# Kernel tuning notes

Measured on AMD Instinct MI355X. Metric: run time of the kernel, lower is better.

The kernel has to match this reference:

```python
import jax, jax.numpy as jnp
import numpy as np

INPUT_SIZE = 20
HIDDEN = 51
OUT = 1
B = 4096
T = 512


def _init_lstm_params(key, in_dim, hid_dim):
    # PyTorch LSTMCell init: U(-1/sqrt(hid), 1/sqrt(hid))
    k = 1.0 / np.sqrt(hid_dim)
    ks = jax.random.split(key, 4)
    W_ih = jax.random.uniform(ks[0], (4 * hid_dim, in_dim), minval=-k, maxval=k, dtype=jnp.float32)
    W_hh = jax.random.uniform(ks[1], (4 * hid_dim, hid_dim), minval=-k, maxval=k, dtype=jnp.float32)
    b_ih = jax.random.uniform(ks[2], (4 * hid_dim,), minval=-k, maxval=k, dtype=jnp.float32)
    b_hh = jax.random.uniform(ks[3], (4 * hid_dim,), minval=-k, maxval=k, dtype=jnp.float32)
    return W_ih, W_hh, b_ih, b_hh


def setup_inputs() -> dict:
    key = jax.random.key(0)
    k_x, k1, k2, k3, k4 = jax.random.split(key, 5)
    x = jax.random.normal(k_x, (B, T, INPUT_SIZE), dtype=jnp.float32)
    W_ih1, W_hh1, b_ih1, b_hh1 = _init_lstm_params(k1, INPUT_SIZE, HIDDEN)
    W_ih2, W_hh2, b_ih2, b_hh2 = _init_lstm_params(k2, HIDDEN, OUT)
    kl = 1.0 / np.sqrt(OUT)
    ka, kb, kc, kd = jax.random.split(k3, 4)
    W_mu = jax.random.uniform(ka, (OUT, OUT), minval=-kl, maxval=kl, dtype=jnp.float32)
    b_mu = jax.random.uniform(kb, (OUT,), minval=-kl, maxval=kl, dtype=jnp.float32)
    W_lv = jax.random.uniform(kc, (OUT, OUT), minval=-kl, maxval=kl, dtype=jnp.float32)
    b_lv = jax.random.uniform(kd, (OUT,), minval=-kl, maxval=kl, dtype=jnp.float32)
    return {
        "x": x,
        "W_ih1": W_ih1, "W_hh1": W_hh1, "b_ih1": b_ih1, "b_hh1": b_hh1,
        "W_ih2": W_ih2, "W_hh2": W_hh2, "b_ih2": b_ih2, "b_hh2": b_hh2,
        "W_mu": W_mu, "b_mu": b_mu, "W_lv": W_lv, "b_lv": b_lv,
    }


def _lstm_cell(x_t, h, c, W_ih, W_hh, b_ih, b_hh):
    # PyTorch LSTMCell: gate order i, f, g, o
    gates = x_t @ W_ih.T + b_ih + h @ W_hh.T + b_hh
    i, f, g, o = jnp.split(gates, 4, axis=-1)
    c_new = jax.nn.sigmoid(f) * c + jax.nn.sigmoid(i) * jnp.tanh(g)
    h_new = jax.nn.sigmoid(o) * jnp.tanh(c_new)
    return h_new, c_new


def reference(x, W_ih1, W_hh1, b_ih1, b_hh1, W_ih2, W_hh2, b_ih2, b_hh2, W_mu, b_mu, W_lv, b_lv):
    bsz = x.shape[0]
    h1 = jnp.zeros((bsz, HIDDEN), dtype=x.dtype)
    c1 = jnp.zeros((bsz, HIDDEN), dtype=x.dtype)
    h2 = jnp.zeros((bsz, OUT), dtype=x.dtype)
    c2 = jnp.zeros((bsz, OUT), dtype=x.dtype)

    def step(carry, x_t):
        h1, c1, h2, c2 = carry
        h1, c1 = _lstm_cell(x_t, h1, c1, W_ih1, W_hh1, b_ih1, b_hh1)
        h2, c2 = _lstm_cell(h1, h2, c2, W_ih2, W_hh2, b_ih2, b_hh2)
        return (h1, c1, h2, c2), h2

    xs = jnp.swapaxes(x, 0, 1)  # [T, B, input_size]
    _, h2_seq = jax.lax.scan(step, (h1, c1, h2, c2), xs)  # h2_seq: [T, B, 1]
    agg = jnp.mean(h2_seq, axis=0)  # [B, 1] mean over time
    mu = agg @ W_mu.T + b_mu
    log_var = agg @ W_lv.T + b_lv
    sigma = jnp.exp(0.5 * log_var)
    lower = mu - 1.96 * sigma
    upper = mu + 1.96 * sigma
    return (lower, mu, upper, log_var)
```

## Files before the change

### kernel.cpp

```cpp
#include <hip/hip_runtime.h>

#define B_TOT 4096
#define T_STEPS 512
#define IN 20
#define HID 51

typedef float f32x4 __attribute__((ext_vector_type(4)));
typedef short s16x8 __attribute__((ext_vector_type(8)));

__device__ __forceinline__ unsigned short f2bf(float f) {
    unsigned int u = __float_as_uint(f);
    unsigned int r = (u + 0x7fffu + ((u >> 16) & 1u)) >> 16;
    return (unsigned short)r;
}

#define L2E  1.4426950408889634f
#define L2E2 2.8853900817779268f

__device__ __forceinline__ float fast_rcp(float x) { return __builtin_amdgcn_rcpf(x); }
__device__ __forceinline__ float sig_p(float p) { return fast_rcp(1.0f + exp2f(p)); }
__device__ __forceinline__ float tanh_q(float q) { return 1.0f - 2.0f * fast_rcp(1.0f + exp2f(q)); }


__global__ __launch_bounds__(512, 2)
void lstm_fused(const float* __restrict__ x,
                const float* __restrict__ Wih1, const float* __restrict__ Whh1,
                const float* __restrict__ bih1, const float* __restrict__ bhh1,
                const float* __restrict__ Wih2, const float* __restrict__ Whh2,
                const float* __restrict__ bih2, const float* __restrict__ bhh2,
                const float* __restrict__ Wmu,  const float* __restrict__ bmu,
                const float* __restrict__ Wlv,  const float* __restrict__ blv,
                float* __restrict__ out)
{
    __shared__ __align__(16) unsigned short vA[2][3][64][8];

    const int tid  = threadIdx.x;
    const int lane = tid & 63;
    const int w    = tid >> 6;
    const int bidx = blockIdx.x;

    const int tbase = (w == 0) ? 0 : (w == 7) ? 12 : 2 * w - 1;
    const int ntile = (w >= 1 && w <= 5) ? 2 : 1;
    const bool isST = (w == 0);
    const bool isL2 = (w == 6);

    s16x8 wfrag[2][3];
    f32x4 binit[2];
    #pragma unroll
    for (int ti = 0; ti < 2; ++ti) {
        const int tau = tbase + ti;
        const int m = lane & 15;
        const bool act = (ti < ntile);
        #pragma unroll
        for (int ks = 0; ks < 3; ++ks) {
            s16x8 f;
            #pragma unroll
            for (int j = 0; j < 8; ++j) {
                int k = ks * 32 + ((lane >> 4) << 3) + j;
                float v = 0.0f;
                if (act) {
                    int g = m & 3, unit = tau * 4 + (m >> 2);
                    if (unit < HID) {
                        int row = g * HID + unit;
                        if (k < IN) v = Wih1[row * IN + k];
                        else if (k >= 32 && k < 32 + HID) v = Whh1[row * HID + (k - 32)];
                        v *= (g == 2) ? L2E2 : -L2E;
                    }
                }
                f[j] = (short)f2bf(v);
            }
            wfrag[ti][ks] = f;
        }
        f32x4 bi = {0.f, 0.f, 0.f, 0.f};
        if (act) {
            int unit = tau * 4 + (lane >> 4);
            if (unit < HID) {
                #pragma unroll
                for (int r = 0; r < 4; ++r)
                    bi[r] = (bih1[r * HID + unit] + bhh1[r * HID + unit]) * ((r == 2) ? L2E2 : -L2E);
            }
        }
        binit[ti] = bi;
    }

    s16x8 l2frag[2];
    f32x4 l2binit = {0.f, 0.f, 0.f, 0.f};
    float whh2g[4] = {0.f, 0.f, 0.f, 0.f};
    if (isL2) {
        const int m = lane & 15;
        #pragma unroll
        for (int ks = 1; ks < 3; ++ks) {
            s16x8 f;
            #pragma unroll
            for (int j = 0; j < 8; ++j) {
                int k = ks * 32 + ((lane >> 4) << 3) + j;
                float v = 0.0f;
                if (m < 4 && k >= 32 && k < 32 + HID)
                    v = Wih2[m * HID + (k - 32)] * ((m == 2) ? L2E2 : -L2E);
                f[j] = (short)f2bf(v);
            }
            l2frag[ks - 1] = f;
        }
        #pragma unroll
        for (int r = 0; r < 4; ++r) {
            float s = (r == 2) ? L2E2 : -L2E;
            whh2g[r]   = Whh2[r] * s;
            l2binit[r] = (bih2[r] + bhh2[r]) * s;
        }
    }

    const float* sp[5];
    int srow[5], sj[5];
    if (isST) {
        #pragma unroll
        for (int i = 0; i < 5; ++i) {
            int e = i * 64 + lane;
            int b = e / IN, m = e % IN;
            sp[i]   = x + ((size_t)(bidx * 16 + b) * T_STEPS) * IN + m;
            srow[i] = ((m >> 3) & 3) * 16 + b;
            sj[i]   = m & 7;
        }
    }

    {
        unsigned short* vz = &vA[0][0][0][0];
        for (int i = tid; i < 2 * 3 * 64 * 8; i += 512) vz[i] = 0;
    }
    __syncthreads();
    float xr[5];
    if (isST) {
        #pragma unroll
        for (int i = 0; i < 5; ++i) {
            vA[0][0][srow[i]][sj[i]] = f2bf(sp[i][0]);
            xr[i] = sp[i][IN];
        }
    }
    __syncthreads();

    float c1[2] = {0.f, 0.f};
    float c2p = 0.f, h2p = 0.f, sum2 = 0.f;

#define STEP(P, tt)                                                              \
    {                                                                            \
        const s16x8 bf0 = *(const s16x8*)&vA[P][0][lane][0];                     \
        const s16x8 bf1 = *(const s16x8*)&vA[P][1][lane][0];                     \
        const s16x8 bf2 = *(const s16x8*)&vA[P][2][lane][0];                     \
        _Pragma("unroll")                                                        \
        for (int ti = 0; ti < 2; ++ti) {                                         \
            if (ti < ntile) {                                                    \
                f32x4 a = binit[ti];                                             \
                a = __builtin_amdgcn_mfma_f32_16x16x32_bf16(wfrag[ti][0], bf0, a, 0, 0, 0); \
                a = __builtin_amdgcn_mfma_f32_16x16x32_bf16(wfrag[ti][1], bf1, a, 0, 0, 0); \
                a = __builtin_amdgcn_mfma_f32_16x16x32_bf16(wfrag[ti][2], bf2, a, 0, 0, 0); \
                float c = sig_p(a[1]) * c1[ti] + sig_p(a[0]) * tanh_q(a[2]);     \
                c1[ti] = c;                                                      \
                float h = sig_p(a[3]) * tanh_q(L2E2 * c);                        \
                int unit = (tbase + ti) * 4 + (lane >> 4);                       \
                int k    = 32 + unit;                                            \
                int b    = lane & 15;                                            \
                vA[(P) ^ 1][k >> 5][(((k >> 3) & 3) << 4) + b][k & 7] = f2bf(h); \
            }                                                                    \
        }                                                                        \
        if (isL2) {                                                              \
            f32x4 a = l2binit;                                                   \
            a = __builtin_amdgcn_mfma_f32_16x16x32_bf16(l2frag[0], bf1, a, 0, 0, 0); \
            a = __builtin_amdgcn_mfma_f32_16x16x32_bf16(l2frag[1], bf2, a, 0, 0, 0); \
            if ((tt) > 0 && lane < 16) {                                         \
                float pi = a[0] + whh2g[0] * h2p;                                \
                float pf = a[1] + whh2g[1] * h2p;                                \
                float pg = a[2] + whh2g[2] * h2p;                                \
                float po = a[3] + whh2g[3] * h2p;                                \
                float c2 = sig_p(pf) * c2p + sig_p(pi) * tanh_q(pg);             \
                c2p = c2;                                                        \
                h2p = sig_p(po) * tanh_q(L2E2 * c2);                             \
                sum2 += h2p;                                                     \
            }                                                                    \
        }                                                                        \
        if (isST) {                                                              \
            const int t2 = ((tt) < T_STEPS - 2) ? (tt) + 2 : T_STEPS - 1;        \
            _Pragma("unroll")                                                    \
            for (int i = 0; i < 5; ++i) {                                        \
                vA[(P) ^ 1][0][srow[i]][sj[i]] = f2bf(xr[i]);                    \
                xr[i] = sp[i][(size_t)t2 * IN];                                  \
            }                                                                    \
        }                                                                        \
        __syncthreads();                                                         \
    }

    for (int t = 0; t < T_STEPS; t += 2) {
        STEP(0, t)
        STEP(1, t + 1)
    }
#undef STEP

    if (isL2) {
        s16x8 bf1 = *(const s16x8*)&vA[0][1][lane][0];
        s16x8 bf2 = *(const s16x8*)&vA[0][2][lane][0];
        f32x4 a = l2binit;
        a = __builtin_amdgcn_mfma_f32_16x16x32_bf16(l2frag[0], bf1, a, 0, 0, 0);
        a = __builtin_amdgcn_mfma_f32_16x16x32_bf16(l2frag[1], bf2, a, 0, 0, 0);
        if (lane < 16) {
            float pi = a[0] + whh2g[0] * h2p;
            float pf = a[1] + whh2g[1] * h2p;
            float pg = a[2] + whh2g[2] * h2p;
            float po = a[3] + whh2g[3] * h2p;
            float c2 = sig_p(pf) * c2p + sig_p(pi) * tanh_q(pg);
            h2p = sig_p(po) * tanh_q(L2E2 * c2);
            sum2 += h2p;

            float agg = sum2 * (1.0f / 512.0f);
            float mu  = Wmu[0] * agg + bmu[0];
            float lv  = Wlv[0] * agg + blv[0];
            float sg  = __expf(0.5f * lv);
            int bg = bidx * 16 + lane;
            out[bg]             = mu - 1.96f * sg;
            out[B_TOT + bg]     = mu;
            out[2 * B_TOT + bg] = mu + 1.96f * sg;
            out[3 * B_TOT + bg] = lv;
        }
    }
}

extern "C" void kernel_launch(void* const* d_in, const int* in_sizes, int n_in,
                              void* d_out, int out_size, void* d_ws, size_t ws_size,
                              hipStream_t stream) {
    const float* x    = (const float*)d_in[0];
    const float* Wih1 = (const float*)d_in[1];
    const float* Whh1 = (const float*)d_in[2];
    const float* bih1 = (const float*)d_in[3];
    const float* bhh1 = (const float*)d_in[4];
    const float* Wih2 = (const float*)d_in[5];
    const float* Whh2 = (const float*)d_in[6];
    const float* bih2 = (const float*)d_in[7];
    const float* bhh2 = (const float*)d_in[8];
    const float* Wmu  = (const float*)d_in[9];
    const float* bmu  = (const float*)d_in[10];
    const float* Wlv  = (const float*)d_in[11];
    const float* blv  = (const float*)d_in[12];
    float* out = (float*)d_out;

    lstm_fused<<<dim3(B_TOT / 16), dim3(512), 0, stream>>>(
        x, Wih1, Whh1, bih1, bhh1, Wih2, Whh2, bih2, bhh2, Wmu, bmu, Wlv, blv, out);
}
```

Before: 505.4 us.

## Halve batch per block to double grid size, and fold tanh scaling into cell state

Each block now handles 8 batch rows instead of 16, so the grid doubles to 512 blocks. This spreads the latency-bound recurrence across more CUs and waves, at the cost of leaving half of each 16-wide MFMA tile idle. The cell state is now kept pre-scaled by 2*log2(e) through a new tanh2_q helper, which drops one multiply per cell. Plain exp2f is replaced with the raw amdgcn exp2 builtin. Fewer staging threads are needed to load x, which adds lane guards.

```diff
diff --git a/kernel.cpp b/kernel.cpp
--- a/kernel.cpp
+++ b/kernel.cpp
@@ -4,6 +4,7 @@
 #define T_STEPS 512
 #define IN 20
 #define HID 51
+#define NB 8
 
 typedef float f32x4 __attribute__((ext_vector_type(4)));
 typedef short s16x8 __attribute__((ext_vector_type(8)));
@@ -18,8 +19,12 @@
 #define L2E2 2.8853900817779268f
 
 __device__ __forceinline__ float fast_rcp(float x) { return __builtin_amdgcn_rcpf(x); }
-__device__ __forceinline__ float sig_p(float p) { return fast_rcp(1.0f + exp2f(p)); }
-__device__ __forceinline__ float tanh_q(float q) { return 1.0f - 2.0f * fast_rcp(1.0f + exp2f(q)); }
+__device__ __forceinline__ float ex2(float x)      { return __builtin_amdgcn_exp2f(x); }
+__device__ __forceinline__ float sig_p(float p)  { return fast_rcp(1.0f + ex2(p)); }
+__device__ __forceinline__ float tanh_q(float q) { return 1.0f - 2.0f * fast_rcp(1.0f + ex2(q)); }
+__device__ __forceinline__ float tanh2_q(float q) {
+    return __builtin_fmaf(fast_rcp(1.0f + ex2(q)), -2.0f * L2E2, L2E2);
+}
 
 
 __global__ __launch_bounds__(512, 2)
@@ -109,16 +114,19 @@
         }
     }
 
-    const float* sp[5];
-    int srow[5], sj[5];
+    const float* sp[3];
+    int srow[3], sj[3];
     if (isST) {
         #pragma unroll
-        for (int i = 0; i < 5; ++i) {
+        for (int i = 0; i < 3; ++i) {
             int e = i * 64 + lane;
-            int b = e / IN, m = e % IN;
-            sp[i]   = x + ((size_t)(bidx * 16 + b) * T_STEPS) * IN + m;
-            srow[i] = ((m >> 3) & 3) * 16 + b;
-            sj[i]   = m & 7;
+            sp[i] = x;  srow[i] = 0;  sj[i] = 0;
+            if (e < NB * IN) {
+                int b = e / IN, m = e % IN;
+                sp[i]   = x + ((size_t)(bidx * NB + b) * T_STEPS) * IN + m;
+                srow[i] = ((m >> 3) & 3) * 16 + b;
+                sj[i]   = m & 7;
+            }
         }
     }
 
@@ -127,18 +135,20 @@
         for (int i = tid; i < 2 * 3 * 64 * 8; i += 512) vz[i] = 0;
     }
     __syncthreads();
-    float xr[5];
+    float xr[3];
     if (isST) {
         #pragma unroll
-        for (int i = 0; i < 5; ++i) {
-            vA[0][0][srow[i]][sj[i]] = f2bf(sp[i][0]);
-            xr[i] = sp[i][IN];
+        for (int i = 0; i < 3; ++i) {
+            if (i < 2 || lane < 32) {
+                vA[0][0][srow[i]][sj[i]] = f2bf(sp[i][0]);
+                xr[i] = sp[i][IN];
+            }
         }
     }
     __syncthreads();
 
-    float c1[2] = {0.f, 0.f};
-    float c2p = 0.f, h2p = 0.f, sum2 = 0.f;
+    float C1[2] = {0.f, 0.f};
+    float C2p = 0.f, h2p = 0.f, sum2 = 0.f;
 
 #define STEP(P, tt)                                                              \
     {                                                                            \
@@ -152,9 +162,9 @@
                 a = __builtin_amdgcn_mfma_f32_16x16x32_bf16(wfrag[ti][0], bf0, a, 0, 0, 0); \
                 a = __builtin_amdgcn_mfma_f32_16x16x32_bf16(wfrag[ti][1], bf1, a, 0, 0, 0); \
                 a = __builtin_amdgcn_mfma_f32_16x16x32_bf16(wfrag[ti][2], bf2, a, 0, 0, 0); \
-                float c = sig_p(a[1]) * c1[ti] + sig_p(a[0]) * tanh_q(a[2]);     \
-                c1[ti] = c;                                                      \
-                float h = sig_p(a[3]) * tanh_q(L2E2 * c);                        \
+                float C = sig_p(a[1]) * C1[ti] + sig_p(a[0]) * tanh2_q(a[2]);    \
+                C1[ti] = C;                                                      \
+                float h = sig_p(a[3]) * tanh_q(C);                               \
                 int unit = (tbase + ti) * 4 + (lane >> 4);                       \
                 int k    = 32 + unit;                                            \
                 int b    = lane & 15;                                            \
@@ -170,18 +180,20 @@
                 float pf = a[1] + whh2g[1] * h2p;                                \
                 float pg = a[2] + whh2g[2] * h2p;                                \
                 float po = a[3] + whh2g[3] * h2p;                                \
-                float c2 = sig_p(pf) * c2p + sig_p(pi) * tanh_q(pg);             \
-                c2p = c2;                                                        \
-                h2p = sig_p(po) * tanh_q(L2E2 * c2);                             \
+                float C2 = sig_p(pf) * C2p + sig_p(pi) * tanh2_q(pg);            \
+                C2p = C2;                                                        \
+                h2p = sig_p(po) * tanh_q(C2);                                    \
                 sum2 += h2p;                                                     \
             }                                                                    \
         }                                                                        \
         if (isST) {                                                              \
             const int t2 = ((tt) < T_STEPS - 2) ? (tt) + 2 : T_STEPS - 1;        \
             _Pragma("unroll")                                                    \
-            for (int i = 0; i < 5; ++i) {                                        \
-                vA[(P) ^ 1][0][srow[i]][sj[i]] = f2bf(xr[i]);                    \
-                xr[i] = sp[i][(size_t)t2 * IN];                                  \
+            for (int i = 0; i < 3; ++i) {                                        \
+                if (i < 2 || lane < 32) {                                        \
+                    vA[(P) ^ 1][0][srow[i]][sj[i]] = f2bf(xr[i]);                \
+                    xr[i] = sp[i][(size_t)t2 * IN];                              \
+                }                                                                \
             }                                                                    \
         }                                                                        \
         __syncthreads();                                                         \
@@ -199,20 +211,20 @@
         f32x4 a = l2binit;
         a = __builtin_amdgcn_mfma_f32_16x16x32_bf16(l2frag[0], bf1, a, 0, 0, 0);
         a = __builtin_amdgcn_mfma_f32_16x16x32_bf16(l2frag[1], bf2, a, 0, 0, 0);
-        if (lane < 16) {
+        if (lane < NB) {
             float pi = a[0] + whh2g[0] * h2p;
             float pf = a[1] + whh2g[1] * h2p;
             float pg = a[2] + whh2g[2] * h2p;
             float po = a[3] + whh2g[3] * h2p;
-            float c2 = sig_p(pf) * c2p + sig_p(pi) * tanh_q(pg);
-            h2p = sig_p(po) * tanh_q(L2E2 * c2);
+            float C2 = sig_p(pf) * C2p + sig_p(pi) * tanh2_q(pg);
+            h2p = sig_p(po) * tanh_q(C2);
             sum2 += h2p;
 
             float agg = sum2 * (1.0f / 512.0f);
             float mu  = Wmu[0] * agg + bmu[0];
             float lv  = Wlv[0] * agg + blv[0];
             float sg  = __expf(0.5f * lv);
-            int bg = bidx * 16 + lane;
+            int bg = bidx * NB + lane;
             out[bg]             = mu - 1.96f * sg;
             out[B_TOT + bg]     = mu;
             out[2 * B_TOT + bg] = mu + 1.96f * sg;
@@ -239,6 +251,6 @@
     const float* blv  = (const float*)d_in[12];
     float* out = (float*)d_out;
 
-    lstm_fused<<<dim3(B_TOT / 16), dim3(512), 0, stream>>>(
+    lstm_fused<<<dim3(B_TOT / NB), dim3(512), 0, stream>>>(
         x, Wih1, Whh1, bih1, bhh1, Wih2, Whh2, bih2, bhh2, Wmu, bmu, Wlv, blv, out);
 }
```

Result: slower. 545.7 us (+8.0%).
